# Kernel optimization log

Hardware: AMD Instinct MI355X
Metric: run time of the kernel (lower is better)

## Reference

```python
import jax, jax.numpy as jnp
from jax import lax
import numpy as np

B, S, D, H = 8, 1024, 512, 8
DH, FF, INNER, K = D // H, 4 * D, 2 * D, 31
SQRT_D = float(np.sqrt(D))  # module scales by sqrt(dim), not sqrt(dim_head)


def _ln(x, g, b, eps=1e-5):
    m = jnp.mean(x, -1, keepdims=True)
    v = jnp.var(x, -1, keepdims=True)
    return (x - m) / jnp.sqrt(v + eps) * g + b


def _swish(x):
    return x * jax.nn.sigmoid(x)


def _ff(x, g, b, w1, b1, w2, b2):
    return _swish(_ln(x, g, b) @ w1 + b1) @ w2 + b2


def _pos_encoding(s, d):
    pos = jnp.arange(s, dtype=jnp.float32)[:, None]
    div = jnp.exp(jnp.arange(0, d, 2, dtype=jnp.float32) * (-np.log(10000.0) / d))
    pe = jnp.zeros((s, d), jnp.float32)
    pe = pe.at[:, 0::2].set(jnp.sin(pos * div))
    pe = pe.at[:, 1::2].set(jnp.cos(pos * div))
    return pe


def _rel_shift(ps):  # (b, h, s, t) Transformer-XL relative shift
    b, h, s, t = ps.shape
    ps = jnp.pad(ps, ((0, 0), (0, 0), (0, 0), (1, 0)))
    return ps.reshape(b, h, t + 1, s)[:, :, 1:].reshape(b, h, s, t)


def _forward(x, ff1_ln_g, ff1_ln_b, ff1_w1, ff1_b1, ff1_w2, ff1_b2,
             attn_ln_g, attn_ln_b, wq, bq, wk, bk, wv, bv, wpos,
             u_bias, v_bias, wo, bo,
             conv_ln_g, conv_ln_b, pw1_w, pw1_b, dw_w, dw_b,
             bn_g, bn_b, bn_mean, bn_var, pw2_w, pw2_b,
             ff2_ln_g, ff2_ln_b, ff2_w1, ff2_b1, ff2_w2, ff2_b2,
             norm_g, norm_b):
    b, s, d = x.shape
    # FF1 half-residual
    x = 0.5 * _ff(x, ff1_ln_g, ff1_ln_b, ff1_w1, ff1_b1, ff1_w2, ff1_b2) + x
    # relative-position multi-head self-attention
    y = _ln(x, attn_ln_g, attn_ln_b)
    q = (y @ wq + bq).reshape(b, s, H, DH)
    k = (y @ wk + bk).reshape(b, s, H, DH)
    v = (y @ wv + bv).reshape(b, s, H, DH)
    pos = (_pos_encoding(s, d) @ wpos).reshape(s, H, DH)  # identical across batch
    score = jnp.einsum('bshd,bthd->bhst', q + u_bias, k)
    pos_score = _rel_shift(jnp.einsum('bshd,thd->bhst', q + v_bias, pos))
    attn = jax.nn.softmax((score + pos_score) / SQRT_D, axis=-1)
    ctx = jnp.einsum('bhst,bthd->bshd', attn, v).reshape(b, s, d)
    x = ctx @ wo + bo + x
    # conformer conv module: LN -> pointwise -> GLU -> depthwise -> BN -> swish -> pointwise
    c = _ln(x, conv_ln_g, conv_ln_b) @ pw1_w + pw1_b  # (b, s, 2*inner)
    a, gate = jnp.split(c, 2, axis=-1)
    z = jnp.transpose(a * jax.nn.sigmoid(gate), (0, 2, 1))  # (b, inner, s)
    z = jnp.pad(z, ((0, 0), (0, 0), (K // 2, K // 2)))  # pad (15, 15) for k=31
    z = lax.conv_general_dilated(z, dw_w[:, None, :], (1,), 'VALID',
                                 dimension_numbers=('NCH', 'OIH', 'NCH'),
                                 feature_group_count=INNER) + dw_b[None, :, None]
    z = (z - bn_mean[None, :, None]) * (bn_g / jnp.sqrt(bn_var + 1e-5))[None, :, None] + bn_b[None, :, None]
    z = _swish(z)
    x = jnp.transpose(z, (0, 2, 1)) @ pw2_w + pw2_b + x
    # FF2 half-residual + final LN
    x = 0.5 * _ff(x, ff2_ln_g, ff2_ln_b, ff2_w1, ff2_b1, ff2_w2, ff2_b2) + x
    return _ln(x, norm_g, norm_b)


def setup_inputs() -> dict:
    key = jax.random.key(0)
    ks = iter(jax.random.split(key, 64))

    def w(shape, scale=0.02):
        return scale * jax.random.normal(next(ks), shape, jnp.float32)

    return {
        'x': jax.random.normal(next(ks), (B, S, D), jnp.float32),
        'ff1_ln_g': jnp.ones(D, jnp.float32), 'ff1_ln_b': jnp.zeros(D, jnp.float32),
        'ff1_w1': w((D, FF)), 'ff1_b1': jnp.zeros(FF, jnp.float32),
        'ff1_w2': w((FF, D)), 'ff1_b2': jnp.zeros(D, jnp.float32),
        'attn_ln_g': jnp.ones(D, jnp.float32), 'attn_ln_b': jnp.zeros(D, jnp.float32),
        'wq': w((D, D)), 'bq': jnp.zeros(D, jnp.float32),
        'wk': w((D, D)), 'bk': jnp.zeros(D, jnp.float32),
        'wv': w((D, D)), 'bv': jnp.zeros(D, jnp.float32),
        'wpos': w((D, D)),
        'u_bias': w((H, DH)), 'v_bias': w((H, DH)),
        'wo': w((D, D)), 'bo': jnp.zeros(D, jnp.float32),
        'conv_ln_g': jnp.ones(D, jnp.float32), 'conv_ln_b': jnp.zeros(D, jnp.float32),
        'pw1_w': w((D, 2 * INNER)), 'pw1_b': jnp.zeros(2 * INNER, jnp.float32),
        'dw_w': w((INNER, K)), 'dw_b': jnp.zeros(INNER, jnp.float32),
        'bn_g': jnp.ones(INNER, jnp.float32), 'bn_b': jnp.zeros(INNER, jnp.float32),
        'bn_mean': jnp.zeros(INNER, jnp.float32), 'bn_var': jnp.ones(INNER, jnp.float32),
        'pw2_w': w((INNER, D)), 'pw2_b': jnp.zeros(D, jnp.float32),
        'ff2_ln_g': jnp.ones(D, jnp.float32), 'ff2_ln_b': jnp.zeros(D, jnp.float32),
        'ff2_w1': w((D, FF)), 'ff2_b1': jnp.zeros(FF, jnp.float32),
        'ff2_w2': w((FF, D)), 'ff2_b2': jnp.zeros(D, jnp.float32),
        'norm_g': jnp.ones(D, jnp.float32), 'norm_b': jnp.zeros(D, jnp.float32),
    }


def reference(x, ff1_ln_g, ff1_ln_b, ff1_w1, ff1_b1, ff1_w2, ff1_b2,
              attn_ln_g, attn_ln_b, wq, bq, wk, bk, wv, bv, wpos,
              u_bias, v_bias, wo, bo,
              conv_ln_g, conv_ln_b, pw1_w, pw1_b, dw_w, dw_b,
              bn_g, bn_b, bn_mean, bn_var, pw2_w, pw2_b,
              ff2_ln_g, ff2_ln_b, ff2_w1, ff2_b1, ff2_w2, ff2_b2,
              norm_g, norm_b):
    return _forward(x, ff1_ln_g, ff1_ln_b, ff1_w1, ff1_b1, ff1_w2, ff1_b2,
                    attn_ln_g, attn_ln_b, wq, bq, wk, bk, wv, bv, wpos,
                    u_bias, v_bias, wo, bo,
                    conv_ln_g, conv_ln_b, pw1_w, pw1_b, dw_w, dw_b,
                    bn_g, bn_b, bn_mean, bn_var, pw2_w, pw2_b,
                    ff2_ln_g, ff2_ln_b, ff2_w1, ff2_b1, ff2_w2, ff2_b2,
                    norm_g, norm_b)
```

## Files before the change

### kernel.cpp

```cpp
#include <hip/hip_runtime.h>
#include <cstdint>
#include <cstddef>

#define B_ 8
#define S_ 1024
#define D_ 512
#define H_ 8
#define DH_ 64
#define FF_ 2048
#define INNER_ 1024
#define NROWS 8192
#define INV_SQRT_D 0.04419417382415922f

typedef __attribute__((ext_vector_type(8))) short bf16x8;
typedef __attribute__((ext_vector_type(4))) float f32x4;
struct alignas(8) short4x { short x, y, z, w; };

__device__ __forceinline__ float sigmoidf_(float x) { return 1.f / (1.f + expf(-x)); }

__device__ __forceinline__ short f2bf(float f) {
  uint32_t u = __float_as_uint(f);
  u += 0x7fff + ((u >> 16) & 1);
  return (short)(u >> 16);
}
__device__ __forceinline__ float bf2f(short s) {
  return __uint_as_float(((uint32_t)(uint16_t)s) << 16);
}

__device__ __forceinline__ void store_out(float* C, size_t i, float v) { C[i] = v; }
__device__ __forceinline__ void store_out(short* C, size_t i, float v) { C[i] = f2bf(v); }

__device__ __forceinline__ void gload_lds16(const void* g, void* lds) {
  __builtin_amdgcn_global_load_lds(
      (const __attribute__((address_space(1))) uint32_t*)g,
      (__attribute__((address_space(3))) uint32_t*)lds, 16, 0, 0);
}

template <typename OutT>
__global__ __launch_bounds__(256) void ln_kernel(const float* __restrict__ in,
    const float* __restrict__ g, const float* __restrict__ b,
    OutT* __restrict__ out) {
  int row = blockIdx.x;
  const float* x = in + (size_t)row * D_;
  OutT* o = out + (size_t)row * D_;
  int t = threadIdx.x;
  float v0 = x[t], v1 = x[t + 256];
  float s = v0 + v1, q = v0 * v0 + v1 * v1;
#pragma unroll
  for (int off = 32; off > 0; off >>= 1) {
    s += __shfl_down(s, off);
    q += __shfl_down(q, off);
  }
  __shared__ float red[8];
  int wid = t >> 6, lane = t & 63;
  if (lane == 0) { red[wid] = s; red[wid + 4] = q; }
  __syncthreads();
  if (t == 0) {
    float S = red[0] + red[1] + red[2] + red[3];
    float Q = red[4] + red[5] + red[6] + red[7];
    float mean = S * (1.f / D_);
    float var = Q * (1.f / D_) - mean * mean;
    red[0] = mean;
    red[1] = rsqrtf(var + 1e-5f);
  }
  __syncthreads();
  float mean = red[0], inv = red[1];
  store_out(o, t, (v0 - mean) * inv * g[t] + b[t]);
  store_out(o, t + 256, (v1 - mean) * inv * g[t + 256] + b[t + 256]);
}

__global__ __launch_bounds__(256) void transpose_bf16_kernel(const float* __restrict__ in,
    short* __restrict__ out, int K, int N) {
  __shared__ float t[32][33];
  int n0 = blockIdx.x << 5, k0 = blockIdx.y << 5;
  int tx = threadIdx.x & 31, ty = threadIdx.x >> 5;
#pragma unroll
  for (int e = 0; e < 4; ++e)
    t[ty + e * 8][tx] = in[(size_t)(k0 + ty + e * 8) * N + n0 + tx];
  __syncthreads();
#pragma unroll
  for (int e = 0; e < 4; ++e)
    out[(size_t)(n0 + ty + e * 8) * K + k0 + tx] = f2bf(t[tx][ty + e * 8]);
}

template <int BN, int EPI, typename OutT>
__global__ __launch_bounds__(256) void mfma_gemm(const short* __restrict__ A,
    const short* __restrict__ Bt, const float* __restrict__ bias,
    const float* __restrict__ res, OutT* __restrict__ C, short* __restrict__ C2,
    const float* __restrict__ bias2, const float* __restrict__ bias3,
    int M, int N, int K) {
  constexpr int NFN = BN / 32;
  __shared__ short As[2][128 * 32];
  __shared__ short Bs[2][BN * 32];
  int tid = threadIdx.x;
  int w = tid >> 6, l = tid & 63;
  int nwg = gridDim.x * gridDim.y;
  int flat = blockIdx.y * gridDim.x + blockIdx.x;
  int W = (flat & 7) * (nwg >> 3) + (flat >> 3);
  int bm = (W / gridDim.x) << 7, bn = (W % gridDim.x) * BN;
  int wr = w >> 1, wc = w & 1;
  f32x4 acc[4][NFN] = {};

  int sr = l >> 2, sc = l & 3;
  int ra0 = (w * 2 + 0) * 16 + sr;
  int ra1 = (w * 2 + 1) * 16 + sr;
  int ga0 = sc ^ ((ra0 >> 1) & 3);
  int ga1 = sc ^ ((ra1 >> 1) & 3);
  const short* a0 = A + (size_t)(bm + ra0) * K + ga0 * 8;
  const short* a1 = A + (size_t)(bm + ra1) * K + ga1 * 8;
  int rb0 = (BN == 128) ? ra0 : (w * 16 + sr);
  int gb0 = sc ^ ((rb0 >> 1) & 3);
  const short* b0 = Bt + (size_t)(bn + rb0) * K + gb0 * 8;
  const short* b1 = Bt + (size_t)(bn + ra1) * K + ga1 * 8;
  int asd0 = (w * 2 + 0) * 512;
  int asd1 = (w * 2 + 1) * 512;
  int bsd0 = (BN == 128) ? asd0 : w * 512;

  int lcol = l & 15, lk = l >> 4;
  int aoff[4], boff[NFN];
#pragma unroll
  for (int m = 0; m < 4; ++m) {
    int r = wr * 64 + m * 16 + lcol;
    aoff[m] = r * 32 + ((lk ^ ((r >> 1) & 3)) << 3);
  }
#pragma unroll
  for (int n = 0; n < NFN; ++n) {
    int r = wc * (BN / 2) + n * 16 + lcol;
    boff[n] = r * 32 + ((lk ^ ((r >> 1) & 3)) << 3);
  }

  int nt = K >> 5;
  gload_lds16(a0, &As[0][asd0]);
  gload_lds16(a1, &As[0][asd1]);
  gload_lds16(b0, &Bs[0][bsd0]);
  if constexpr (BN == 128) gload_lds16(b1, &Bs[0][asd1]);
  __syncthreads();

  for (int t = 0; t < nt; ++t) {
    int cur = t & 1;
    if (t + 1 < nt) {
      int k1 = (t + 1) << 5;
      gload_lds16(a0 + k1, &As[cur ^ 1][asd0]);
      gload_lds16(a1 + k1, &As[cur ^ 1][asd1]);
      gload_lds16(b0 + k1, &Bs[cur ^ 1][bsd0]);
      if constexpr (BN == 128) gload_lds16(b1 + k1, &Bs[cur ^ 1][asd1]);
    }
    bf16x8 af[4], bfr[NFN];
#pragma unroll
    for (int m = 0; m < 4; ++m) af[m] = *(const bf16x8*)(&As[cur][aoff[m]]);
#pragma unroll
    for (int n = 0; n < NFN; ++n) bfr[n] = *(const bf16x8*)(&Bs[cur][boff[n]]);
#pragma unroll
    for (int m = 0; m < 4; ++m)
#pragma unroll
      for (int n = 0; n < NFN; ++n)
        acc[m][n] = __builtin_amdgcn_mfma_f32_16x16x32_bf16(af[m], bfr[n], acc[m][n], 0, 0, 0);
    __syncthreads();
  }

  int lrow = (l >> 4) << 2;
#pragma unroll
  for (int m = 0; m < 4; ++m) {
    int row0 = bm + wr * 64 + m * 16 + lrow;
#pragma unroll
    for (int n = 0; n < NFN; ++n) {
      int col = bn + wc * (BN / 2) + n * 16 + lcol;
      float bv = bias ? bias[col] : 0.f;
      if (EPI == 5) {
        short4x o;
        o.x = f2bf(acc[m][n][0] + bv);
        o.y = f2bf(acc[m][n][1] + bv);
        o.z = f2bf(acc[m][n][2] + bv);
        o.w = f2bf(acc[m][n][3] + bv);
        size_t tidx = ((size_t)(row0 >> 10) * 512 + col) * 1024 + (row0 & 1023);
        *(short4x*)((short*)C + tidx) = o;
      } else if (EPI == 4) {
#pragma unroll
        for (int r = 0; r < 4; ++r) {
          size_t idx = (size_t)(row0 + r) * N + col;
          float v = acc[m][n][r] + bv;
          ((short*)C)[idx] = f2bf(v + bias2[col]);
          C2[idx] = f2bf(v + bias3[col]);
        }
      } else {
#pragma unroll
        for (int r = 0; r < 4; ++r) {
          size_t idx = (size_t)(row0 + r) * N + col;
          float v = acc[m][n][r] + bv;
          if (EPI == 1) v = v * sigmoidf_(v);
          else if (EPI == 2) v = 0.5f * v + res[idx];
          else if (EPI == 3) v = v + res[idx];
          store_out(C, idx, v);
        }
      }
    }
  }
}

__global__ __launch_bounds__(256) void pe_kernel(short* __restrict__ pe) {
  int t = blockIdx.x, i = threadIdx.x;
  float freq = expf((float)(2 * i) * (-9.2103403719761836f / 512.f));
  float arg = (float)t * freq;
  pe[(size_t)t * D_ + 2 * i] = f2bf(sinf(arg));
  pe[(size_t)t * D_ + 2 * i + 1] = f2bf(cosf(arg));
}

__global__ __launch_bounds__(256) void attn_pos_mfma(const short* __restrict__ Qb,
    const short* __restrict__ Pos, short* __restrict__ Out, int bh0) {
  __shared__ short Qs[128 * 64];
  __shared__ short Ks[128 * 64];
  int tid = threadIdx.x;
  int w = tid >> 6, l = tid & 63;
  int z = blockIdx.z;
  int bh = bh0 + z, b = bh >> 3, h = bh & 7;
  int bi = blockIdx.y << 7, bj = blockIdx.x << 7;
  int srow = w * 8 + (l >> 3);
  int sch = l & 7;
#pragma unroll
  for (int cc = 0; cc < 4; ++cc) {
    int r = cc * 32 + srow;
    int g = sch ^ (r & 7);
    gload_lds16(Qb + (size_t)(b * S_ + bi + r) * D_ + h * DH_ + g * 8, Qs + (cc * 32 + w * 8) * 64);
    gload_lds16(Pos + (size_t)(bj + r) * D_ + h * DH_ + g * 8, Ks + (cc * 32 + w * 8) * 64);
  }
  __syncthreads();
  int wr = w >> 1, wc = w & 1;
  int lcol = l & 15, lk = l >> 4;
  bf16x8 qf[4][2], kf[4][2];
#pragma unroll
  for (int m = 0; m < 4; ++m)
#pragma unroll
    for (int ks = 0; ks < 2; ++ks) {
      int r = wr * 64 + m * 16 + lcol;
      int c = ks * 4 + lk;
      qf[m][ks] = *(const bf16x8*)(Qs + r * 64 + ((c ^ (r & 7)) << 3));
    }
#pragma unroll
  for (int n = 0; n < 4; ++n)
#pragma unroll
    for (int ks = 0; ks < 2; ++ks) {
      int r = wc * 64 + n * 16 + lcol;
      int c = ks * 4 + lk;
      kf[n][ks] = *(const bf16x8*)(Ks + r * 64 + ((c ^ (r & 7)) << 3));
    }
  f32x4 acc[4][4] = {};
#pragma unroll
  for (int ks = 0; ks < 2; ++ks)
#pragma unroll
    for (int m = 0; m < 4; ++m)
#pragma unroll
      for (int n = 0; n < 4; ++n)
        acc[m][n] = __builtin_amdgcn_mfma_f32_16x16x32_bf16(qf[m][ks], kf[n][ks], acc[m][n], 0, 0, 0);
  int lrow = (l >> 4) << 2;
  short* Oz = Out + (size_t)z * S_ * S_;
#pragma unroll
  for (int m = 0; m < 4; ++m)
#pragma unroll
    for (int r = 0; r < 4; ++r) {
      int iG = bi + wr * 64 + m * 16 + lrow + r;
#pragma unroll
      for (int n = 0; n < 4; ++n) {
        int tG = bj + wc * 64 + n * 16 + lcol;
        short val = f2bf(acc[m][n][r]);
        if (tG >= S_ - 1 - iG)
          Oz[(size_t)iG * S_ + (tG - (S_ - 1 - iG))] = val;
        else if (iG >= 1)
          Oz[(size_t)(iG - 1) * S_ + (tG + iG + 1)] = val;
        if (tG == 0 && iG < S_ - 1)
          Oz[(size_t)iG * S_ + iG + 1] = 0;
      }
    }
}

__global__ __launch_bounds__(512) void attn_fused(const short* __restrict__ qu,
    const short* __restrict__ kk, const short* __restrict__ vT,
    const short* __restrict__ Psh, short* __restrict__ ctx, int bh0) {
  __shared__ short Ks[2][64 * 64];
  __shared__ short Vs[2][64 * 64];
  __shared__ short Ps[128 * 64];
  int tid = threadIdx.x;
  int w = tid >> 6, l = tid & 63;
  int z = blockIdx.y;
  int bh = bh0 + z, b = bh >> 3, h = bh & 7;
  int i0 = blockIdx.x << 7;
  bf16x8 qf0, qf1;
  {
    const short* qrow = qu + (size_t)(b * S_ + i0 + w * 16 + (l & 15)) * D_ + h * DH_ + ((l >> 4) << 3);
    qf0 = *(const bf16x8*)(qrow);
    qf1 = *(const bf16x8*)(qrow + 32);
  }
  f32x4 po[4] = {};
  float mrow[4], lrw[4];
  int gi[4];
#pragma unroll
  for (int r = 0; r < 4; ++r) {
    mrow[r] = -1e30f;
    lrw[r] = 0.f;
    gi[r] = i0 + w * 16 + ((l >> 4) << 2) + r;
  }
  const short* prow0 = Psh + (size_t)z * S_ * S_ + (size_t)gi[0] * S_ + (l & 15);
  const short* prow1 = prow0 + S_;
  const short* prow2 = prow1 + S_;
  const short* prow3 = prow2 + S_;

  int srw = (w << 3) + (l >> 3);
  int sg = (l & 7) ^ (srw & 7);
  const short* ksrc = kk + (size_t)(b * S_) * D_ + h * DH_ + (sg << 3);
  const short* vsrc = vT + (size_t)(b * 512 + h * DH_ + srw) * 1024 + (sg << 3);
  int sdst = (w << 3) * 64;

#define STAGE_KV(jt, buf)                                                  \
  {                                                                        \
    int j0_ = (jt) << 6;                                                   \
    gload_lds16(ksrc + (size_t)(j0_ + srw) * D_, &Ks[buf][sdst]);          \
    gload_lds16(vsrc + j0_, &Vs[buf][sdst]);                               \
  }

  float pvc[4][4], pvn[4][4];
#define PLOADF(jt, dst)                                                    \
  {                                                                        \
    int j0_ = (jt) << 6;                                                   \
    _Pragma("unroll") for (int n_ = 0; n_ < 4; ++n_) {                     \
      dst[n_][0] = bf2f(prow0[j0_ + (n_ << 4)]);                           \
      dst[n_][1] = bf2f(prow1[j0_ + (n_ << 4)]);                           \
      dst[n_][2] = bf2f(prow2[j0_ + (n_ << 4)]);                           \
      dst[n_][3] = bf2f(prow3[j0_ + (n_ << 4)]);                           \
    }                                                                      \
  }

  STAGE_KV(0, 0);
  PLOADF(0, pvc);
  __syncthreads();

  for (int jt = 0; jt < 16; ++jt) {
    int buf = jt & 1;
    if (jt < 15) {
      STAGE_KV(jt + 1, buf ^ 1);
      PLOADF(jt + 1, pvn);
    }
    f32x4 sc[4] = {};
#pragma unroll
    for (int ks = 0; ks < 2; ++ks)
#pragma unroll
      for (int n = 0; n < 4; ++n) {
        int rj = (n << 4) + (l & 15);
        int ck = (ks << 2) + (l >> 4);
        bf16x8 kf = *(const bf16x8*)(&Ks[buf][rj * 64 + ((ck ^ (rj & 7)) << 3)]);
        sc[n] = __builtin_amdgcn_mfma_f32_16x16x32_bf16(ks == 0 ? qf0 : qf1, kf, sc[n], 0, 0, 0);
      }
    float pm[4];
#pragma unroll
    for (int r = 0; r < 4; ++r) pm[r] = -1e30f;
#pragma unroll
    for (int n = 0; n < 4; ++n)
#pragma unroll
      for (int r = 0; r < 4; ++r) {
        float v = (sc[n][r] + pvc[n][r]) * INV_SQRT_D;
        sc[n][r] = v;
        pm[r] = fmaxf(pm[r], v);
      }
#pragma unroll
    for (int r = 0; r < 4; ++r)
#pragma unroll
      for (int off = 1; off < 16; off <<= 1) pm[r] = fmaxf(pm[r], __shfl_xor(pm[r], off));
    float psum[4];
#pragma unroll
    for (int r = 0; r < 4; ++r) {
      float mn = fmaxf(mrow[r], pm[r]);
      float f = __expf(mrow[r] - mn);
      mrow[r] = mn;
      lrw[r] *= f;
#pragma unroll
      for (int n = 0; n < 4; ++n) po[n][r] *= f;
      psum[r] = 0.f;
    }
#pragma unroll
    for (int n = 0; n < 4; ++n)
#pragma unroll
      for (int r = 0; r < 4; ++r) {
        float p = __expf(sc[n][r] - mrow[r]);
        psum[r] += p;
        int rr = (w << 4) + ((l >> 4) << 2) + r;
        int c = (n << 4) + (l & 15);
        Ps[rr * 64 + (((c >> 3) ^ (rr & 7)) << 3) + (c & 7)] = f2bf(p);
      }
#pragma unroll
    for (int r = 0; r < 4; ++r) {
#pragma unroll
      for (int off = 1; off < 16; off <<= 1) psum[r] += __shfl_xor(psum[r], off);
      lrw[r] += psum[r];
    }
    int rr2 = (w << 4) + (l & 15);
    bf16x8 pa[2];
#pragma unroll
    for (int ks = 0; ks < 2; ++ks) {
      int ck = (ks << 2) + (l >> 4);
      pa[ks] = *(const bf16x8*)(&Ps[rr2 * 64 + ((ck ^ (rr2 & 7)) << 3)]);
    }
#pragma unroll
    for (int ks = 0; ks < 2; ++ks)
#pragma unroll
      for (int n = 0; n < 4; ++n) {
        int rd = (n << 4) + (l & 15);
        int ck = (ks << 2) + (l >> 4);
        bf16x8 vf = *(const bf16x8*)(&Vs[buf][rd * 64 + ((ck ^ (rd & 7)) << 3)]);
        po[n] = __builtin_amdgcn_mfma_f32_16x16x32_bf16(pa[ks], vf, po[n], 0, 0, 0);
      }
    __syncthreads();
    if (jt < 15) {
#pragma unroll
      for (int n = 0; n < 4; ++n)
#pragma unroll
        for (int r = 0; r < 4; ++r) pvc[n][r] = pvn[n][r];
    }
  }
  short* Cz = ctx + (size_t)b * S_ * D_ + h * DH_;
#pragma unroll
  for (int r = 0; r < 4; ++r) {
    float inv = 1.f / lrw[r];
#pragma unroll
    for (int n = 0; n < 4; ++n)
      Cz[(size_t)gi[r] * D_ + (n << 4) + (l & 15)] = f2bf(po[n][r] * inv);
  }
#undef STAGE_KV
#undef PLOADF
}

__global__ __launch_bounds__(256) void glu_kernel(const short* __restrict__ hbuf,
                                                  short* __restrict__ z) {
  size_t idx4 = ((size_t)blockIdx.x * 256 + threadIdx.x) << 2;
  size_t row = idx4 >> 10, c = idx4 & 1023;
  short4x a4 = *(const short4x*)(hbuf + row * 2048 + c);
  short4x g4 = *(const short4x*)(hbuf + row * 2048 + 1024 + c);
  short4x o;
  o.x = f2bf(bf2f(a4.x) * sigmoidf_(bf2f(g4.x)));
  o.y = f2bf(bf2f(a4.y) * sigmoidf_(bf2f(g4.y)));
  o.z = f2bf(bf2f(a4.z) * sigmoidf_(bf2f(g4.z)));
  o.w = f2bf(bf2f(a4.w) * sigmoidf_(bf2f(g4.w)));
  *(short4x*)(z + idx4) = o;
}

#define CTS 32
__global__ __launch_bounds__(256) void dwconv_kernel(const short* __restrict__ z,
    const float* __restrict__ w, const float* __restrict__ wb,
    const float* __restrict__ bng, const float* __restrict__ bnb,
    const float* __restrict__ bnm, const float* __restrict__ bnv,
    short* __restrict__ out) {
  int c = (blockIdx.z << 8) + threadIdx.x;
  int b = blockIdx.y;
  int s0 = blockIdx.x * CTS;
  float wr[31];
#pragma unroll
  for (int kk = 0; kk < 31; ++kk) wr[kk] = w[c * 31 + kk];
  float zv[CTS + 30];
#pragma unroll
  for (int e = 0; e < CTS + 30; ++e) {
    int sr = s0 - 15 + e;
    zv[e] = (sr >= 0 && sr < S_) ? bf2f(z[((size_t)(b * S_ + sr) << 10) + c]) : 0.f;
  }
  float scale = bng[c] * rsqrtf(bnv[c] + 1e-5f);
  float shift = bnb[c] - bnm[c] * scale;
  float bias = wb[c];
#pragma unroll
  for (int s = 0; s < CTS; ++s) {
    float acc = 0.f;
#pragma unroll
    for (int kk = 0; kk < 31; ++kk) acc += zv[s + kk] * wr[kk];
    float v = (acc + bias) * scale + shift;
    v = v * sigmoidf_(v);
    out[((size_t)(b * S_ + s0 + s) << 10) + c] = f2bf(v);
  }
}

extern "C" void kernel_launch(void* const* d_in, const int* in_sizes, int n_in,
                              void* d_out, int out_size, void* d_ws, size_t ws_size,
                              hipStream_t stream) {
  const float* x_in = (const float*)d_in[0];
  const float* ff1_ln_g = (const float*)d_in[1];
  const float* ff1_ln_b = (const float*)d_in[2];
  const float* ff1_w1 = (const float*)d_in[3];
  const float* ff1_b1 = (const float*)d_in[4];
  const float* ff1_w2 = (const float*)d_in[5];
  const float* ff1_b2 = (const float*)d_in[6];
  const float* attn_ln_g = (const float*)d_in[7];
  const float* attn_ln_b = (const float*)d_in[8];
  const float* wq = (const float*)d_in[9];
  const float* bq = (const float*)d_in[10];
  const float* wk = (const float*)d_in[11];
  const float* bk = (const float*)d_in[12];
  const float* wv = (const float*)d_in[13];
  const float* bv = (const float*)d_in[14];
  const float* wpos = (const float*)d_in[15];
  const float* u_bias = (const float*)d_in[16];
  const float* v_bias = (const float*)d_in[17];
  const float* wo = (const float*)d_in[18];
  const float* bo = (const float*)d_in[19];
  const float* conv_ln_g = (const float*)d_in[20];
  const float* conv_ln_b = (const float*)d_in[21];
  const float* pw1_w = (const float*)d_in[22];
  const float* pw1_b = (const float*)d_in[23];
  const float* dw_w = (const float*)d_in[24];
  const float* dw_b = (const float*)d_in[25];
  const float* bn_g = (const float*)d_in[26];
  const float* bn_b = (const float*)d_in[27];
  const float* bn_mean = (const float*)d_in[28];
  const float* bn_var = (const float*)d_in[29];
  const float* pw2_w = (const float*)d_in[30];
  const float* pw2_b = (const float*)d_in[31];
  const float* ff2_ln_g = (const float*)d_in[32];
  const float* ff2_ln_b = (const float*)d_in[33];
  const float* ff2_w1 = (const float*)d_in[34];
  const float* ff2_b1 = (const float*)d_in[35];
  const float* ff2_w2 = (const float*)d_in[36];
  const float* ff2_b2 = (const float*)d_in[37];
  const float* norm_g = (const float*)d_in[38];
  const float* norm_b = (const float*)d_in[39];

  char* wsb = (char*)d_ws;
  float* xb = (float*)(wsb);
  short* yb16 = (short*)(wsb + (16ull << 20));
  short* qu16 = (short*)(wsb + (24ull << 20));
  short* qv16 = (short*)(wsb + (32ull << 20));
  short* k16 = (short*)(wsb + (40ull << 20));
  short* vT16 = (short*)(wsb + (48ull << 20));
  short* ctx16 = (short*)(wsb + (56ull << 20));
  short* pos16 = (short*)(wsb + (64ull << 20));
  short* wt = (short*)(wsb + (65ull << 20));
  short* Pb16 = (short*)(wsb + (80ull << 20));
  short* hb16 = (short*)(wsb + (80ull << 20));
  short* zb16 = (short*)(wsb + (112ull << 20));
  short* cb16 = (short*)(wsb + (128ull << 20));
  short* peb16 = ctx16;

  short* ff1w1t = wt;
  short* ff1w2t = ff1w1t + 2048 * 512;
  short* wqt = ff1w2t + 512 * 2048;
  short* wkt = wqt + 512 * 512;
  short* wvt = wkt + 512 * 512;
  short* wot = wvt + 512 * 512;
  short* wpost = wot + 512 * 512;
  short* pw1t = wpost + 512 * 512;
  short* pw2t = pw1t + 2048 * 512;
  short* ff2w1t = pw2t + 512 * 1024;
  short* ff2w2t = ff2w1t + 2048 * 512;

  dim3 blk(256);

  transpose_bf16_kernel<<<dim3(64, 16), blk, 0, stream>>>(ff1_w1, ff1w1t, 512, 2048);
  transpose_bf16_kernel<<<dim3(16, 64), blk, 0, stream>>>(ff1_w2, ff1w2t, 2048, 512);
  transpose_bf16_kernel<<<dim3(16, 16), blk, 0, stream>>>(wq, wqt, 512, 512);
  transpose_bf16_kernel<<<dim3(16, 16), blk, 0, stream>>>(wk, wkt, 512, 512);
  transpose_bf16_kernel<<<dim3(16, 16), blk, 0, stream>>>(wv, wvt, 512, 512);
  transpose_bf16_kernel<<<dim3(16, 16), blk, 0, stream>>>(wo, wot, 512, 512);
  transpose_bf16_kernel<<<dim3(16, 16), blk, 0, stream>>>(wpos, wpost, 512, 512);
  transpose_bf16_kernel<<<dim3(64, 16), blk, 0, stream>>>(pw1_w, pw1t, 512, 2048);
  transpose_bf16_kernel<<<dim3(16, 32), blk, 0, stream>>>(pw2_w, pw2t, 1024, 512);
  transpose_bf16_kernel<<<dim3(64, 16), blk, 0, stream>>>(ff2_w1, ff2w1t, 512, 2048);
  transpose_bf16_kernel<<<dim3(16, 64), blk, 0, stream>>>(ff2_w2, ff2w2t, 2048, 512);

  ln_kernel<short><<<NROWS, blk, 0, stream>>>(x_in, ff1_ln_g, ff1_ln_b, yb16);
  mfma_gemm<128, 1, short><<<dim3(FF_ / 128, NROWS / 128), blk, 0, stream>>>(yb16, ff1w1t, ff1_b1, nullptr, hb16, nullptr, nullptr, nullptr, NROWS, FF_, D_);
  mfma_gemm<64, 2, float><<<dim3(D_ / 64, NROWS / 128), blk, 0, stream>>>(hb16, ff1w2t, ff1_b2, x_in, xb, nullptr, nullptr, nullptr, NROWS, D_, FF_);

  ln_kernel<short><<<NROWS, blk, 0, stream>>>(xb, attn_ln_g, attn_ln_b, yb16);
  mfma_gemm<64, 4, short><<<dim3(D_ / 64, NROWS / 128), blk, 0, stream>>>(yb16, wqt, bq, nullptr, qu16, qv16, u_bias, v_bias, NROWS, D_, D_);
  mfma_gemm<64, 0, short><<<dim3(D_ / 64, NROWS / 128), blk, 0, stream>>>(yb16, wkt, bk, nullptr, k16, nullptr, nullptr, nullptr, NROWS, D_, D_);
  mfma_gemm<64, 5, short><<<dim3(D_ / 64, NROWS / 128), blk, 0, stream>>>(yb16, wvt, bv, nullptr, vT16, nullptr, nullptr, nullptr, NROWS, D_, D_);
  pe_kernel<<<S_, blk, 0, stream>>>(peb16);
  mfma_gemm<64, 0, short><<<dim3(D_ / 64, S_ / 128), blk, 0, stream>>>(peb16, wpost, nullptr, nullptr, pos16, nullptr, nullptr, nullptr, S_, D_, D_);

  const int CH = 32;
  for (int c = 0; c < 64 / CH; ++c) {
    int bh0 = c * CH;
    attn_pos_mfma<<<dim3(8, 8, CH), blk, 0, stream>>>(qv16, pos16, Pb16, bh0);
    attn_fused<<<dim3(S_ / 128, CH), dim3(512), 0, stream>>>(qu16, k16, vT16, Pb16, ctx16, bh0);
  }
  mfma_gemm<64, 3, float><<<dim3(D_ / 64, NROWS / 128), blk, 0, stream>>>(ctx16, wot, bo, xb, xb, nullptr, nullptr, nullptr, NROWS, D_, D_);

  ln_kernel<short><<<NROWS, blk, 0, stream>>>(xb, conv_ln_g, conv_ln_b, yb16);
  mfma_gemm<128, 0, short><<<dim3(2 * INNER_ / 128, NROWS / 128), blk, 0, stream>>>(yb16, pw1t, pw1_b, nullptr, hb16, nullptr, nullptr, nullptr, NROWS, 2 * INNER_, D_);
  glu_kernel<<<NROWS * INNER_ / 1024, blk, 0, stream>>>(hb16, zb16);
  dwconv_kernel<<<dim3(S_ / CTS, B_, 4), blk, 0, stream>>>(zb16, dw_w, dw_b, bn_g, bn_b, bn_mean, bn_var, cb16);
  mfma_gemm<64, 3, float><<<dim3(D_ / 64, NROWS / 128), blk, 0, stream>>>(cb16, pw2t, pw2_b, xb, xb, nullptr, nullptr, nullptr, NROWS, D_, INNER_);

  ln_kernel<short><<<NROWS, blk, 0, stream>>>(xb, ff2_ln_g, ff2_ln_b, yb16);
  mfma_gemm<128, 1, short><<<dim3(FF_ / 128, NROWS / 128), blk, 0, stream>>>(yb16, ff2w1t, ff2_b1, nullptr, hb16, nullptr, nullptr, nullptr, NROWS, FF_, D_);
  mfma_gemm<64, 2, float><<<dim3(D_ / 64, NROWS / 128), blk, 0, stream>>>(hb16, ff2w2t, ff2_b2, xb, xb, nullptr, nullptr, nullptr, NROWS, D_, FF_);

  ln_kernel<float><<<NROWS, blk, 0, stream>>>(xb, norm_g, norm_b, (float*)d_out);
}
```

Measured before the change: 512.2 us.

## Triple-buffer GEMM LDS staging with explicit vmcnt waits and raw barriers

Measured after the change: 514.0 us. About the same (+0.4%).

```diff
diff --git a/kernel.cpp b/kernel.cpp
--- a/kernel.cpp
+++ b/kernel.cpp
@@ -90,8 +90,8 @@
     const float* __restrict__ bias2, const float* __restrict__ bias3,
     int M, int N, int K) {
   constexpr int NFN = BN / 32;
-  __shared__ short As[2][128 * 32];
-  __shared__ short Bs[2][BN * 32];
+  __shared__ short As[3][128 * 32];
+  __shared__ short Bs[3][BN * 32];
   int tid = threadIdx.x;
   int w = tid >> 6, l = tid & 63;
   int nwg = gridDim.x * gridDim.y;
@@ -129,22 +129,29 @@
     boff[n] = r * 32 + ((lk ^ ((r >> 1) & 3)) << 3);
   }
 
+#define STAGE_T(kk, bb)                                             \
+  {                                                                 \
+    gload_lds16(a0 + (kk), &As[bb][asd0]);                          \
+    gload_lds16(a1 + (kk), &As[bb][asd1]);                          \
+    gload_lds16(b0 + (kk), &Bs[bb][bsd0]);                          \
+    if constexpr (BN == 128) gload_lds16(b1 + (kk), &Bs[bb][asd1]); \
+  }
+
   int nt = K >> 5;
-  gload_lds16(a0, &As[0][asd0]);
-  gload_lds16(a1, &As[0][asd1]);
-  gload_lds16(b0, &Bs[0][bsd0]);
-  if constexpr (BN == 128) gload_lds16(b1, &Bs[0][asd1]);
-  __syncthreads();
-
+  STAGE_T(0, 0);
+  STAGE_T(32, 1);
+
+  int cur = 0, nxt = 2;
   for (int t = 0; t < nt; ++t) {
-    int cur = t & 1;
-    if (t + 1 < nt) {
-      int k1 = (t + 1) << 5;
-      gload_lds16(a0 + k1, &As[cur ^ 1][asd0]);
-      gload_lds16(a1 + k1, &As[cur ^ 1][asd1]);
-      gload_lds16(b0 + k1, &Bs[cur ^ 1][bsd0]);
-      if constexpr (BN == 128) gload_lds16(b1 + k1, &Bs[cur ^ 1][asd1]);
-    }
+    int kpre = ((t + 2 < nt) ? (t + 2) : (nt - 1)) << 5;
+    STAGE_T(kpre, nxt);
+    if constexpr (BN == 128)
+      asm volatile("s_waitcnt vmcnt(8)" ::: "memory");
+    else
+      asm volatile("s_waitcnt vmcnt(6)" ::: "memory");
+    __builtin_amdgcn_sched_barrier(0);
+    __builtin_amdgcn_s_barrier();
+    __builtin_amdgcn_sched_barrier(0);
     bf16x8 af[4], bfr[NFN];
 #pragma unroll
     for (int m = 0; m < 4; ++m) af[m] = *(const bf16x8*)(&As[cur][aoff[m]]);
@@ -155,8 +162,12 @@
 #pragma unroll
       for (int n = 0; n < NFN; ++n)
         acc[m][n] = __builtin_amdgcn_mfma_f32_16x16x32_bf16(af[m], bfr[n], acc[m][n], 0, 0, 0);
-    __syncthreads();
-  }
+    __builtin_amdgcn_s_barrier();
+    __builtin_amdgcn_sched_barrier(0);
+    cur = (cur == 2) ? 0 : cur + 1;
+    nxt = (nxt == 2) ? 0 : nxt + 1;
+  }
+#undef STAGE_T
 
   int lrow = (l >> 4) << 2;
 #pragma unroll
```
